# Performance work log

Measured on AMD Instinct MI355X. Metric: run time of the kernel, lower is better.

The kernel has to match this reference:

```python
import jax, jax.numpy as jnp
import numpy as np

B, D, N, K = 16, 128, 4096, 1024


def setup_inputs() -> dict:
    key = jax.random.key(0)
    k1, k2 = jax.random.split(key)
    ze = jax.random.normal(k1, (B, D, N), dtype=jnp.float32)
    emb = jax.random.normal(k2, (K, D), dtype=jnp.float32)
    return {"ze": ze, "emb": emb}


def reference(ze, emb):
    """VQ forward: nearest-codebook quantization with straight-through estimator.

    ze:  (B, D, N) encoder latents (D = n_latent_dim, N = timesteps)
    emb: (K, D) codebook (stop-gradient applied, matching StopGrad on emb)
    returns zq_rg: (B, D, N) quantized latents; gradient flows straight to ze
    (ReplaceGrad: zq gets zero grad, ze gets the output grad).
    """
    emb_sg = jax.lax.stop_gradient(emb)
    # Squared L2 distance via expansion, avoiding the (B, D, K, N) broadcast:
    # d2[b,k,n] = ||ze[b,:,n]||^2 + ||emb[k]||^2 - 2 <ze[b,:,n], emb[k]>
    ze_sq = jnp.sum(ze * ze, axis=1)            # (B, N)
    emb_sq = jnp.sum(emb_sg * emb_sg, axis=1)   # (K,)
    dot = jnp.einsum('bdn,kd->bkn', ze, emb_sg)  # (B, K, N)
    d2 = ze_sq[:, None, :] + emb_sq[None, :, None] - 2.0 * dot
    ind = jnp.argmin(d2, axis=1)                # (B, N) nearest codebook index
    zq = jnp.transpose(jnp.take(emb_sg, ind, axis=0), (0, 2, 1))  # (B, D, N)
    # ReplaceGrad straight-through: value of zq, gradient routed to ze.
    zq_rg = ze + jax.lax.stop_gradient(zq - ze)
    return zq_rg
```

## Files before the change

### kernel.cpp

```cpp
#include <hip/hip_runtime.h>
#include <hip/hip_bf16.h>
#include <math.h>

#define BB 16
#define DD 128
#define NN 4096
#define KK 1024
#define TAU 0.28f

typedef __attribute__((ext_vector_type(8))) short short8;
typedef __attribute__((ext_vector_type(4))) float f32x4;

static __device__ __forceinline__ unsigned short f32_bf16_rne(float f) {
    unsigned u = __float_as_uint(f);
    u += 0x7FFF + ((u >> 16) & 1);
    return (unsigned short)(u >> 16);
}
static __device__ __forceinline__ unsigned umin32(unsigned a, unsigned b) { return a < b ? a : b; }
static __device__ __forceinline__ unsigned umax32(unsigned a, unsigned b) { return a > b ? a : b; }

__global__ void emb_sq_kernel(const float* __restrict__ emb,
                              float* __restrict__ e2) {
    int k = blockIdx.x * 256 + threadIdx.x;
    if (k >= KK) return;
    const float4* row = reinterpret_cast<const float4*>(emb + (size_t)k * DD);
    float a0 = 0.f, a1 = 0.f, a2 = 0.f, a3 = 0.f;
#pragma unroll
    for (int i = 0; i < DD / 16; ++i) {
        float4 v0 = row[i * 4 + 0];
        float4 v1 = row[i * 4 + 1];
        float4 v2 = row[i * 4 + 2];
        float4 v3 = row[i * 4 + 3];
        a0 += v0.x * v0.x + v0.y * v0.y + v0.z * v0.z + v0.w * v0.w;
        a1 += v1.x * v1.x + v1.y * v1.y + v1.z * v1.z + v1.w * v1.w;
        a2 += v2.x * v2.x + v2.y * v2.y + v2.z * v2.z + v2.w * v2.w;
        a3 += v3.x * v3.x + v3.y * v3.y + v3.z * v3.z + v3.w * v3.w;
    }
    e2[k] = (a0 + a1) + (a2 + a3);
}

__global__ void emb_pack_kernel(const float* __restrict__ emb,
                                short* __restrict__ epk) {
    int g = blockIdx.x * 256 + threadIdx.x;
    int lane = g & 63;
    int s    = (g >> 6) & 3;
    int t    = g >> 8;
    int k = t * 16 + (lane & 15);
    int d = s * 32 + ((lane >> 4) & 3) * 8;
    const float* src = emb + (size_t)k * DD + d;
    short8 h;
#pragma unroll
    for (int j = 0; j < 8; ++j) h[j] = (short)f32_bf16_rne(-2.0f * src[j]);
    *reinterpret_cast<short8*>(epk + (size_t)g * 8) = h;
}

#define CEU(a, b) { unsigned lo_ = umin32(a, b), hi_ = umax32(a, b); (a) = lo_; (b) = hi_; }

__global__ __launch_bounds__(256, 4)
void vq_mfma(const float* __restrict__ ze, const float* __restrict__ emb,
             const short* __restrict__ epk, const float* __restrict__ e2,
             float* __restrict__ out) {
    __shared__ unsigned kbuf[2][64][4];
    __shared__ int winner_s[64];
    __shared__ int rlist[64];
    __shared__ int rcnt;
    __shared__ float ew[64][DD + 1];

    const int lane = threadIdx.x & 63;
    const int wave = threadIdx.x >> 6;
    const int b    = blockIdx.x >> 6;
    const int n0b  = (blockIdx.x & 63) * 64;
    const int cgrp = wave & 1;
    const int khalf = wave >> 1;
    const int col0w = n0b + cgrp * 32;
    const float* zb = ze + (size_t)b * DD * NN;

    const int nq = lane & 15;
    const int dq = (lane >> 4) & 3;

    if (threadIdx.x == 0) rcnt = 0;

    short8 zf[2][4];
    float z2p[2] = {0.f, 0.f};
#pragma unroll
    for (int cg = 0; cg < 2; ++cg) {
        const int col = col0w + cg * 16 + nq;
#pragma unroll
        for (int s = 0; s < 4; ++s) {
#pragma unroll
            for (int j = 0; j < 8; ++j) {
                int d = s * 32 + dq * 8 + j;
                float z = zb[(size_t)d * NN + col];
                zf[cg][s][j] = (short)f32_bf16_rne(z);
                z2p[cg] += z * z;
            }
        }
    }
#pragma unroll
    for (int cg = 0; cg < 2; ++cg) {
        z2p[cg] += __shfl_xor(z2p[cg], 16);
        z2p[cg] += __shfl_xor(z2p[cg], 32);
        z2p[cg] += 1.0f;
    }

    unsigned K1[2], K2[2], K3[2], K4[2];
#pragma unroll
    for (int cg = 0; cg < 2; ++cg) { K1[cg] = K2[cg] = K3[cg] = K4[cg] = 0xFFFFFFFFu; }

    const int t0 = khalf * 32;

#define FRAG(T, S) \
    (*reinterpret_cast<const short8*>(epk + (((size_t)((T) * 4 + (S)) * 64 + lane) << 3)))

    short8 aC0 = FRAG(t0, 0), aC1 = FRAG(t0, 1), aC2 = FRAG(t0, 2), aC3 = FRAG(t0, 3);
    float4 evC = *reinterpret_cast<const float4*>(e2 + t0 * 16 + dq * 4);

#pragma unroll 2
    for (int tt = 0; tt < 32; ++tt) {
        short8 aN0, aN1, aN2, aN3; float4 evN;
        if (tt < 31) {
            const int tn = t0 + tt + 1;
            aN0 = FRAG(tn, 0); aN1 = FRAG(tn, 1);
            aN2 = FRAG(tn, 2); aN3 = FRAG(tn, 3);
            evN = *reinterpret_cast<const float4*>(e2 + tn * 16 + dq * 4);
            asm volatile("s_waitcnt vmcnt(5)" ::: "memory");
        } else {
            asm volatile("s_waitcnt vmcnt(0)" ::: "memory");
        }
        __builtin_amdgcn_sched_barrier(0);

        f32x4 acc0 = {evC.x + z2p[0], evC.y + z2p[0], evC.z + z2p[0], evC.w + z2p[0]};
        f32x4 acc1 = {evC.x + z2p[1], evC.y + z2p[1], evC.z + z2p[1], evC.w + z2p[1]};
#define STEP(AF, S) \
        acc0 = __builtin_amdgcn_mfma_f32_16x16x32_bf16(AF, zf[0][S], acc0, 0, 0, 0); \
        acc1 = __builtin_amdgcn_mfma_f32_16x16x32_bf16(AF, zf[1][S], acc1, 0, 0, 0);
        STEP(aC0, 0) STEP(aC1, 1) STEP(aC2, 2) STEP(aC3, 3)
#undef STEP

        const unsigned kbase = (unsigned)((t0 + tt) * 16 + dq * 4);
#pragma unroll
        for (int cg = 0; cg < 2; ++cg) {
            const f32x4 a = (cg == 0) ? acc0 : acc1;
#pragma unroll
            for (int r = 0; r < 4; ++r) {
                unsigned x = (__float_as_uint(a[r]) & 0xFFFFFC00u) | (kbase + r);
                unsigned t1;
                t1 = umin32(K1[cg], x); x = umax32(K1[cg], x); K1[cg] = t1;
                t1 = umin32(K2[cg], x); x = umax32(K2[cg], x); K2[cg] = t1;
                t1 = umin32(K3[cg], x); x = umax32(K3[cg], x); K3[cg] = t1;
                K4[cg] = umin32(K4[cg], x);
            }
        }
        aC0 = aN0; aC1 = aN1; aC2 = aN2; aC3 = aN3; evC = evN;
    }
#undef FRAG

#pragma unroll
    for (int cg = 0; cg < 2; ++cg) {
#pragma unroll
        for (int off = 16; off < 64; off <<= 1) {
            unsigned B1 = __shfl_xor(K1[cg], off);
            unsigned B2 = __shfl_xor(K2[cg], off);
            unsigned B3 = __shfl_xor(K3[cg], off);
            unsigned B4 = __shfl_xor(K4[cg], off);
            CEU(K1[cg], B1) CEU(K2[cg], B2) CEU(K3[cg], B3) CEU(K4[cg], B4)
            CEU(K3[cg], B1) CEU(K4[cg], B2)
            CEU(K2[cg], K3[cg])
            CEU(K4[cg], B1)
            CEU(K3[cg], K4[cg])
        }
    }

    if (lane < 32) {
        const int cgid = lane >> 4;
        const int bc = cgrp * 32 + lane;
        kbuf[khalf][bc][0] = cgid ? K1[1] : K1[0];
        kbuf[khalf][bc][1] = cgid ? K2[1] : K2[0];
        kbuf[khalf][bc][2] = cgid ? K3[1] : K3[0];
        kbuf[khalf][bc][3] = cgid ? K4[1] : K4[0];
    }
    __syncthreads();

    if (wave == 0) {
        unsigned A1 = kbuf[0][lane][0], A2 = kbuf[0][lane][1];
        unsigned A3 = kbuf[0][lane][2], A4 = kbuf[0][lane][3];
        unsigned B1 = kbuf[1][lane][0], B2 = kbuf[1][lane][1];
        unsigned B3 = kbuf[1][lane][2], B4 = kbuf[1][lane][3];
        CEU(A1, B1) CEU(A2, B2) CEU(A3, B3) CEU(A4, B4)
        CEU(A3, B1) CEU(A4, B2)
        CEU(A2, A3)
        CEU(A4, B1)
        CEU(A3, A4)
        const float M1 = __uint_as_float(A1 & 0xFFFFFC00u);
        const float M2 = __uint_as_float(A2 & 0xFFFFFC00u);
        const bool trig = (M2 - M1) < TAU;
        winner_s[lane] = (int)(A1 & 0x3FFu);
        kbuf[0][lane][0] = A1; kbuf[0][lane][1] = A2;
        kbuf[0][lane][2] = A3; kbuf[0][lane][3] = A4;
        const unsigned long long mask = __ballot(trig);
        if (trig) {
            const int idx = __popcll(mask & ((1ull << lane) - 1ull));
            rlist[idx] = lane;
        }
        if (lane == 0) rcnt = (int)__popcll(mask);
    }
    __syncthreads();

    {
        const int rc = rcnt;
        for (int j = wave; j < rc; j += 4) {
            const int c = rlist[j];
            const int coln = n0b + c;
            const int I0 = (int)(kbuf[0][c][0] & 0x3FFu);
            const int I1 = (int)(kbuf[0][c][1] & 0x3FFu);
            const int I2 = (int)(kbuf[0][c][2] & 0x3FFu);
            const int I3 = (int)(kbuf[0][c][3] & 0x3FFu);
            double s0 = 0.0, s1 = 0.0, s2 = 0.0, s3 = 0.0;
#pragma unroll
            for (int h = 0; h < 2; ++h) {
                const int d = h * 64 + lane;
                const double zv = (double)zb[(size_t)d * NN + coln];
                double q;
                q = zv - (double)emb[(size_t)I0 * DD + d]; s0 += q * q;
                q = zv - (double)emb[(size_t)I1 * DD + d]; s1 += q * q;
                q = zv - (double)emb[(size_t)I2 * DD + d]; s2 += q * q;
                q = zv - (double)emb[(size_t)I3 * DD + d]; s3 += q * q;
            }
#pragma unroll
            for (int off = 1; off < 64; off <<= 1) {
                s0 += __shfl_xor(s0, off);
                s1 += __shfl_xor(s1, off);
                s2 += __shfl_xor(s2, off);
                s3 += __shfl_xor(s3, off);
            }
            int best = I0; double db = s0;
            if (s1 < db || (s1 == db && I1 < best)) { db = s1; best = I1; }
            if (s2 < db || (s2 == db && I2 < best)) { db = s2; best = I2; }
            if (s3 < db || (s3 == db && I3 < best)) { db = s3; best = I3; }
            if (lane == 0) winner_s[c] = best;
        }
    }
    __syncthreads();

#pragma unroll 4
    for (int r = wave * 16; r < wave * 16 + 16; ++r) {
        const int idx = winner_s[r];
        ew[r][lane]      = emb[(size_t)idx * DD + lane];
        ew[r][lane + 64] = emb[(size_t)idx * DD + lane + 64];
    }
    __syncthreads();

#pragma unroll 4
    for (int dd = 0; dd < 32; ++dd) {
        const int d = wave * 32 + dd;
        const int coln = n0b + lane;
        const float zv = zb[(size_t)d * NN + coln];
        const float evv = ew[lane][d];
        out[((size_t)b * DD + d) * NN + coln] = zv + (evv - zv);
    }
}

extern "C" void kernel_launch(void* const* d_in, const int* in_sizes, int n_in,
                              void* d_out, int out_size, void* d_ws, size_t ws_size,
                              hipStream_t stream) {
    (void)in_sizes; (void)n_in; (void)out_size; (void)ws_size;
    const float* ze  = (const float*)d_in[0];
    const float* emb = (const float*)d_in[1];
    float*       out = (float*)d_out;

    char* ws = (char*)d_ws;
    short* epk = (short*)ws;
    float* e2  = (float*)(ws + (size_t)KK * DD * 2);

    emb_sq_kernel<<<KK / 256, 256, 0, stream>>>(emb, e2);
    emb_pack_kernel<<<(KK * DD / 8) / 256, 256, 0, stream>>>(emb, epk);
    vq_mfma<<<(BB * NN) / 64, 256, 0, stream>>>(ze, emb, epk, e2, out);
}
```

Before: 54.47 us.

## Shrink block tile to 32 columns and split codebook across four waves

Each block now handles 32 timestep columns instead of 64, and each of its four waves scans a quarter of the codebook (16 tiles) rather than splitting by column group and codebook half. The launch doubles to 2048 blocks, and wave 0 merges four top-4 lists instead of two. The goal is more blocks for better occupancy and load balance and a shorter serial MFMA loop per wave. In exchange, every block loads the full codebook fragments for only 32 columns, which halves codebook reuse per block and adds merge work. The output epilogue is remapped so that half-waves cover 32 columns.

Result: slower. 57.80 us (+6.1%).

```diff
diff --git a/kernel.cpp b/kernel.cpp
--- a/kernel.cpp
+++ b/kernel.cpp
@@ -55,36 +55,37 @@
 }
 
 #define CEU(a, b) { unsigned lo_ = umin32(a, b), hi_ = umax32(a, b); (a) = lo_; (b) = hi_; }
+#define MRG9(A1, A2, A3, A4, B1, B2, B3, B4) \
+    CEU(A1, B1) CEU(A2, B2) CEU(A3, B3) CEU(A4, B4) \
+    CEU(A3, B1) CEU(A4, B2) \
+    CEU(A2, A3) \
+    CEU(A4, B1) \
+    CEU(A3, A4)
 
 __global__ __launch_bounds__(256, 4)
 void vq_mfma(const float* __restrict__ ze, const float* __restrict__ emb,
              const short* __restrict__ epk, const float* __restrict__ e2,
              float* __restrict__ out) {
-    __shared__ unsigned kbuf[2][64][4];
-    __shared__ int winner_s[64];
-    __shared__ int rlist[64];
+    __shared__ unsigned kbuf[4][32][4];
+    __shared__ int winner_s[32];
+    __shared__ int rlist[32];
     __shared__ int rcnt;
-    __shared__ float ew[64][DD + 1];
+    __shared__ float ew[32][DD + 1];
 
     const int lane = threadIdx.x & 63;
     const int wave = threadIdx.x >> 6;
-    const int b    = blockIdx.x >> 6;
-    const int n0b  = (blockIdx.x & 63) * 64;
-    const int cgrp = wave & 1;
-    const int khalf = wave >> 1;
-    const int col0w = n0b + cgrp * 32;
+    const int b    = blockIdx.x >> 7;
+    const int n0b  = (blockIdx.x & 127) * 32;
     const float* zb = ze + (size_t)b * DD * NN;
 
     const int nq = lane & 15;
     const int dq = (lane >> 4) & 3;
 
-    if (threadIdx.x == 0) rcnt = 0;
-
     short8 zf[2][4];
     float z2p[2] = {0.f, 0.f};
 #pragma unroll
     for (int cg = 0; cg < 2; ++cg) {
-        const int col = col0w + cg * 16 + nq;
+        const int col = n0b + cg * 16 + nq;
 #pragma unroll
         for (int s = 0; s < 4; ++s) {
 #pragma unroll
@@ -107,7 +108,7 @@
 #pragma unroll
     for (int cg = 0; cg < 2; ++cg) { K1[cg] = K2[cg] = K3[cg] = K4[cg] = 0xFFFFFFFFu; }
 
-    const int t0 = khalf * 32;
+    const int t0 = wave * 16;
 
 #define FRAG(T, S) \
     (*reinterpret_cast<const short8*>(epk + (((size_t)((T) * 4 + (S)) * 64 + lane) << 3)))
@@ -116,9 +117,9 @@
     float4 evC = *reinterpret_cast<const float4*>(e2 + t0 * 16 + dq * 4);
 
 #pragma unroll 2
-    for (int tt = 0; tt < 32; ++tt) {
+    for (int tt = 0; tt < 16; ++tt) {
         short8 aN0, aN1, aN2, aN3; float4 evN;
-        if (tt < 31) {
+        if (tt < 15) {
             const int tn = t0 + tt + 1;
             aN0 = FRAG(tn, 0); aN1 = FRAG(tn, 1);
             aN2 = FRAG(tn, 2); aN3 = FRAG(tn, 3);
@@ -163,44 +164,50 @@
             unsigned B2 = __shfl_xor(K2[cg], off);
             unsigned B3 = __shfl_xor(K3[cg], off);
             unsigned B4 = __shfl_xor(K4[cg], off);
-            CEU(K1[cg], B1) CEU(K2[cg], B2) CEU(K3[cg], B3) CEU(K4[cg], B4)
-            CEU(K3[cg], B1) CEU(K4[cg], B2)
-            CEU(K2[cg], K3[cg])
-            CEU(K4[cg], B1)
-            CEU(K3[cg], K4[cg])
+            MRG9(K1[cg], K2[cg], K3[cg], K4[cg], B1, B2, B3, B4)
         }
     }
 
     if (lane < 32) {
         const int cgid = lane >> 4;
-        const int bc = cgrp * 32 + lane;
-        kbuf[khalf][bc][0] = cgid ? K1[1] : K1[0];
-        kbuf[khalf][bc][1] = cgid ? K2[1] : K2[0];
-        kbuf[khalf][bc][2] = cgid ? K3[1] : K3[0];
-        kbuf[khalf][bc][3] = cgid ? K4[1] : K4[0];
+        kbuf[wave][lane][0] = cgid ? K1[1] : K1[0];
+        kbuf[wave][lane][1] = cgid ? K2[1] : K2[0];
+        kbuf[wave][lane][2] = cgid ? K3[1] : K3[0];
+        kbuf[wave][lane][3] = cgid ? K4[1] : K4[0];
     }
     __syncthreads();
 
     if (wave == 0) {
-        unsigned A1 = kbuf[0][lane][0], A2 = kbuf[0][lane][1];
-        unsigned A3 = kbuf[0][lane][2], A4 = kbuf[0][lane][3];
-        unsigned B1 = kbuf[1][lane][0], B2 = kbuf[1][lane][1];
-        unsigned B3 = kbuf[1][lane][2], B4 = kbuf[1][lane][3];
-        CEU(A1, B1) CEU(A2, B2) CEU(A3, B3) CEU(A4, B4)
-        CEU(A3, B1) CEU(A4, B2)
-        CEU(A2, A3)
-        CEU(A4, B1)
-        CEU(A3, A4)
+        const int c = lane & 31;
+        unsigned A1 = kbuf[0][c][0], A2 = kbuf[0][c][1];
+        unsigned A3 = kbuf[0][c][2], A4 = kbuf[0][c][3];
+        {
+            unsigned B1 = kbuf[1][c][0], B2 = kbuf[1][c][1];
+            unsigned B3 = kbuf[1][c][2], B4 = kbuf[1][c][3];
+            MRG9(A1, A2, A3, A4, B1, B2, B3, B4)
+        }
+        {
+            unsigned B1 = kbuf[2][c][0], B2 = kbuf[2][c][1];
+            unsigned B3 = kbuf[2][c][2], B4 = kbuf[2][c][3];
+            MRG9(A1, A2, A3, A4, B1, B2, B3, B4)
+        }
+        {
+            unsigned B1 = kbuf[3][c][0], B2 = kbuf[3][c][1];
+            unsigned B3 = kbuf[3][c][2], B4 = kbuf[3][c][3];
+            MRG9(A1, A2, A3, A4, B1, B2, B3, B4)
+        }
         const float M1 = __uint_as_float(A1 & 0xFFFFFC00u);
         const float M2 = __uint_as_float(A2 & 0xFFFFFC00u);
-        const bool trig = (M2 - M1) < TAU;
-        winner_s[lane] = (int)(A1 & 0x3FFu);
-        kbuf[0][lane][0] = A1; kbuf[0][lane][1] = A2;
-        kbuf[0][lane][2] = A3; kbuf[0][lane][3] = A4;
+        const bool trig = (lane < 32) && ((M2 - M1) < TAU);
+        if (lane < 32) {
+            winner_s[c] = (int)(A1 & 0x3FFu);
+            kbuf[0][c][0] = A1; kbuf[0][c][1] = A2;
+            kbuf[0][c][2] = A3; kbuf[0][c][3] = A4;
+        }
         const unsigned long long mask = __ballot(trig);
         if (trig) {
             const int idx = __popcll(mask & ((1ull << lane) - 1ull));
-            rlist[idx] = lane;
+            rlist[idx] = c;
         }
         if (lane == 0) rcnt = (int)__popcll(mask);
     }
@@ -242,21 +249,25 @@
     }
     __syncthreads();
 
-#pragma unroll 4
-    for (int r = wave * 16; r < wave * 16 + 16; ++r) {
+#pragma unroll 2
+    for (int rr = 0; rr < 8; ++rr) {
+        const int r = wave * 8 + rr;
         const int idx = winner_s[r];
         ew[r][lane]      = emb[(size_t)idx * DD + lane];
         ew[r][lane + 64] = emb[(size_t)idx * DD + lane + 64];
     }
     __syncthreads();
 
+    {
+        const int c = lane & 31;
+        const int coln = n0b + c;
 #pragma unroll 4
-    for (int dd = 0; dd < 32; ++dd) {
-        const int d = wave * 32 + dd;
-        const int coln = n0b + lane;
-        const float zv = zb[(size_t)d * NN + coln];
-        const float evv = ew[lane][d];
-        out[((size_t)b * DD + d) * NN + coln] = zv + (evv - zv);
+        for (int dd = 0; dd < 16; ++dd) {
+            const int d = wave * 32 + dd * 2 + (lane >> 5);
+            const float zv = zb[(size_t)d * NN + coln];
+            const float evv = ew[c][d];
+            out[((size_t)b * DD + d) * NN + coln] = zv + (evv - zv);
+        }
     }
 }
 
@@ -274,5 +285,5 @@
 
     emb_sq_kernel<<<KK / 256, 256, 0, stream>>>(emb, e2);
     emb_pack_kernel<<<(KK * DD / 8) / 256, 256, 0, stream>>>(emb, epk);
-    vq_mfma<<<(BB * NN) / 64, 256, 0, stream>>>(ze, emb, epk, e2, out);
-}
+    vq_mfma<<<(BB * NN) / 32, 256, 0, stream>>>(ze, emb, epk, e2, out);
+}
```
